# Kernel optimization log

Hardware: AMD Instinct MI355X
Metric: run time of the kernel (lower is better)

Reference implementation:

```python
import jax, jax.numpy as jnp
import numpy as np

D_MODEL = 512
BATCH_A = 8192
MAX_MATCHES = 16
N_B = 100000
D_HID = 2 * D_MODEL  # 1024
D_IN = 2 * D_MODEL   # concat([a, mean_b])


def setup_inputs() -> dict:
    key = jax.random.key(0)
    ks = jax.random.split(key, 10)
    table_a_emb = jax.random.normal(ks[0], (BATCH_A, D_MODEL), dtype=jnp.float32)
    table_b_emb = jax.random.normal(ks[1], (N_B, D_MODEL), dtype=jnp.float32)
    # padded neighbor lists; negative values mark padding / no-match
    match_indices = jax.random.randint(ks[2], (BATCH_A, MAX_MATCHES), -5, N_B, dtype=jnp.int64)
    s_in = 1.0 / np.sqrt(D_IN)
    s_h = 1.0 / np.sqrt(D_HID)
    W_in = jax.random.uniform(ks[3], (D_IN, D_HID), jnp.float32, -s_in, s_in)
    b_in = jax.random.uniform(ks[4], (D_HID,), jnp.float32, -s_in, s_in)
    W_h = jax.random.uniform(ks[5], (D_HID, D_HID), jnp.float32, -s_h, s_h)
    b_h = jax.random.uniform(ks[6], (D_HID,), jnp.float32, -s_h, s_h)
    W_out = jax.random.uniform(ks[7], (D_HID, D_MODEL), jnp.float32, -s_h, s_h)
    b_out = jax.random.uniform(ks[8], (D_MODEL,), jnp.float32, -s_h, s_h)
    return {"table_a_emb": table_a_emb, "table_b_emb": table_b_emb,
            "match_indices": match_indices, "W_in": W_in, "b_in": b_in,
            "W_h": W_h, "b_h": b_h, "W_out": W_out, "b_out": b_out}


def reference(table_a_emb, table_b_emb, match_indices, W_in, b_in, W_h, b_h, W_out, b_out):
    mask = match_indices >= 0                                   # [B, M]
    safe_idx = jnp.where(mask, match_indices, 0)
    gathered = table_b_emb[safe_idx] * mask[..., None].astype(table_b_emb.dtype)  # [B, M, D]
    counts = mask.sum(axis=-1)                                  # [B]
    denom = jnp.maximum(counts, 1).astype(table_b_emb.dtype)[:, None]
    agg_b = gathered.sum(axis=1) / denom                        # [B, D] masked mean
    combined = jnp.concatenate([table_a_emb, agg_b], axis=-1)   # [B, 2D]
    h = jax.nn.relu(combined @ W_in + b_in)
    h = jax.nn.relu(h @ W_h + b_h)
    out = h @ W_out + b_out                                     # [B, D]
    # rows with zero valid matches emit zeros, not MLP(concat(a, 0))
    return jnp.where((counts > 0)[:, None], out, jnp.zeros_like(out))
```

## Files before the change

### kernel.cpp

```cpp
#include <hip/hip_runtime.h>

#define DM 512
#define DI 1024
#define MM 16

typedef __attribute__((ext_vector_type(4))) float f32x4;
typedef __attribute__((ext_vector_type(8))) short short8;
typedef __attribute__((ext_vector_type(8))) unsigned short ushort8;

__device__ __forceinline__ unsigned short f2bf(float x) {
  union { float f; unsigned u; } c; c.f = x;
  unsigned r = (c.u + 0x7fffu + ((c.u >> 16) & 1u)) >> 16;
  return (unsigned short)r;
}

__device__ __forceinline__ void gload_lds16(const void* g, void* l) {
  __builtin_amdgcn_global_load_lds(
      (const __attribute__((address_space(1))) unsigned int*)g,
      (__attribute__((address_space(3))) unsigned int*)l, 16, 0, 0);
}

__device__ __forceinline__ void wt_tile(const float* __restrict__ W,
                                        unsigned short* __restrict__ Wt,
                                        int K, int N, int bx, int by,
                                        float (*tile)[33], int tx, int ty) {
  #pragma unroll
  for (int i = ty; i < 32; i += 8)
    tile[i][tx] = W[(size_t)(by + i) * N + bx + tx];
  __syncthreads();
  #pragma unroll
  for (int i = ty; i < 32; i += 8)
    Wt[(size_t)(bx + i) * K + by + tx] = f2bf(tile[tx][i]);
}

__global__ __launch_bounds__(256)
void prep_kernel(const float* __restrict__ Aemb,
                 const float* __restrict__ Bemb,
                 const int* __restrict__ midx,
                 const float* __restrict__ W_in,
                 const float* __restrict__ W_h,
                 const float* __restrict__ W_out,
                 unsigned short* __restrict__ X,
                 int* __restrict__ counts,
                 unsigned short* __restrict__ Wt_in,
                 unsigned short* __restrict__ Wt_h,
                 unsigned short* __restrict__ Wt_out) {
  __shared__ float tile[32][33];
  const int b = blockIdx.x;
  const int tx = threadIdx.x & 31, ty = threadIdx.x >> 5;
  if (b < 1024) {
    wt_tile(W_in, Wt_in, 1024, 1024, (b & 31) * 32, (b >> 5) * 32, tile, tx, ty);
    return;
  } else if (b < 2048) {
    int lb = b - 1024;
    wt_tile(W_h, Wt_h, 1024, 1024, (lb & 31) * 32, (lb >> 5) * 32, tile, tx, ty);
    return;
  } else if (b < 2560) {
    int lb = b - 2048;
    wt_tile(W_out, Wt_out, 1024, 512, (lb & 15) * 32, (lb >> 4) * 32, tile, tx, ty);
    return;
  }
  int row = __builtin_amdgcn_readfirstlane((b - 2560) * 4 + (threadIdx.x >> 6));
  int l = threadIdx.x & 63;
  float acc[8] = {0,0,0,0,0,0,0,0};
  int cnt = 0;
  const int* ip = midx + row * MM;
  #pragma unroll
  for (int m = 0; m < MM; ++m) {
    int id = ip[m];
    if (id >= 0) {
      ++cnt;
      const f32x4* p = (const f32x4*)(Bemb + (size_t)id * DM) + l * 2;
      f32x4 u = p[0], v = p[1];
      acc[0]+=u[0]; acc[1]+=u[1]; acc[2]+=u[2]; acc[3]+=u[3];
      acc[4]+=v[0]; acc[5]+=v[1]; acc[6]+=v[2]; acc[7]+=v[3];
    }
  }
  float inv = 1.0f / (float)(cnt > 0 ? cnt : 1);
  const f32x4* pa = (const f32x4*)(Aemb + (size_t)row * DM) + l * 2;
  f32x4 a0 = pa[0], a1 = pa[1];
  ushort8 va, vb;
  va[0]=f2bf(a0[0]); va[1]=f2bf(a0[1]); va[2]=f2bf(a0[2]); va[3]=f2bf(a0[3]);
  va[4]=f2bf(a1[0]); va[5]=f2bf(a1[1]); va[6]=f2bf(a1[2]); va[7]=f2bf(a1[3]);
  #pragma unroll
  for (int i = 0; i < 8; ++i) vb[i] = f2bf(acc[i] * inv);
  *(ushort8*)(X + (size_t)row * DI + l * 8) = va;
  *(ushort8*)(X + (size_t)row * DI + DM + l * 8) = vb;
  if (l == 0) counts[row] = cnt;
}

__global__ __launch_bounds__(512, 2)
void gemm8_kernel(const unsigned short* __restrict__ A,
                  const unsigned short* __restrict__ Bt,
                  const float* __restrict__ bias,
                  unsigned short* __restrict__ C) {
  extern __shared__ __align__(16) char smem[];
  const int t = threadIdx.x;
  const int l = t & 63, w = t >> 6;
  const int wr = w >> 2, wc = w & 3;
  const int f = blockIdx.y * gridDim.x + blockIdx.x;
  const int swzid = (f & 7) * 32 + (f >> 3);
  const int bx = swzid & 7, by = swzid >> 3;
  const int blockM = by * 256, blockN = bx * 128;
  const unsigned short* __restrict__ Ab = A + (size_t)blockM * 1024;
  const unsigned short* __restrict__ Bb = Bt + (size_t)blockN * 1024;
  const int r = l & 15, ko = (l >> 4) * 8;
  const int swz = (r & 7) << 4;
  const int strow = t >> 3;
  const int stcolh = ((((t & 7) * 16) ^ ((strow & 7) << 4)) >> 1);

  f32x4 acc[8][2];
  #pragma unroll
  for (int m = 0; m < 8; ++m) {
    acc[m][0] = (f32x4){0.f,0.f,0.f,0.f};
    acc[m][1] = (f32x4){0.f,0.f,0.f,0.f};
  }

#define ST_A(BASE, KT, CH)                                                    \
  gload_lds16(Ab + (size_t)((CH)*64 + strow) * 1024 + ((KT)<<6) + stcolh,     \
              smem + (BASE) + (CH)*8192 + t*16);
#define ST_B(BASE, KT, CB)                                                    \
  gload_lds16(Bb + (size_t)((CB)*64 + strow) * 1024 + ((KT)<<6) + stcolh,     \
              smem + (BASE) + 32768 + (CB)*8192 + t*16);
#define ST_QM0B(BASE, KT) { ST_A(BASE,KT,0) ST_A(BASE,KT,2) ST_B(BASE,KT,0) ST_B(BASE,KT,1) }
#define ST_QM1(BASE, KT)  { ST_A(BASE,KT,1) ST_A(BASE,KT,3) }

#define WAIT_VM(N) { asm volatile("s_waitcnt vmcnt(" #N ")" ::: "memory");    \
                     __builtin_amdgcn_sched_barrier(0); }
#define WAIT_LGKM() { asm volatile("s_waitcnt lgkmcnt(0)" ::: "memory");      \
                      __builtin_amdgcn_sched_barrier(0); }
#define BAR() { __builtin_amdgcn_s_barrier();                                 \
                __builtin_amdgcn_sched_barrier(0); }

  short8 aF[4][2], bF[2][2];

#define LDA(MF4, KK, BASE, QM)                                                \
  aF[MF4][KK] = *(const short8*)(smem + (BASE) +                              \
      ((((wr*128 + ((QM)*4+(MF4))*16 + r) * 128) + ((KK)*32 + ko)*2) ^ swz));
#define LDB(NF, KK, BASE)                                                     \
  bF[NF][KK] = *(const short8*)(smem + (BASE) + 32768 +                       \
      ((((wc*32 + (NF)*16 + r) * 128) + ((KK)*32 + ko)*2) ^ swz));

#define MFMA16(QM)                                                            \
  __builtin_amdgcn_s_setprio(1);                                              \
  _Pragma("unroll") for (int mf4 = 0; mf4 < 4; ++mf4)                         \
    _Pragma("unroll") for (int kk = 0; kk < 2; ++kk)                          \
      _Pragma("unroll") for (int nf = 0; nf < 2; ++nf)                        \
        acc[(QM)*4+mf4][nf] = __builtin_amdgcn_mfma_f32_16x16x32_bf16(        \
            aF[mf4][kk], bF[nf][kk], acc[(QM)*4+mf4][nf], 0, 0, 0);           \
  __builtin_amdgcn_s_setprio(0);

#define DS_A(BASE, QM) _Pragma("unroll")                                      \
  for (int mf4 = 0; mf4 < 4; ++mf4) { LDA(mf4,0,BASE,QM) LDA(mf4,1,BASE,QM) }
#define DS_B(BASE) { LDB(0,0,BASE) LDB(0,1,BASE) LDB(1,0,BASE) LDB(1,1,BASE) }

  ST_QM0B(0, 0) ST_QM1(0, 0)
  ST_QM0B(49152, 1) ST_QM1(49152, 1)
  WAIT_VM(8) BAR()

  { DS_A(0,0) DS_B(0)
    WAIT_LGKM() MFMA16(0)
    WAIT_VM(6) BAR() }
  { DS_A(0,1)
    ST_QM0B(0, 2)
    WAIT_LGKM() MFMA16(1)
    WAIT_VM(6) BAR() }

  #pragma unroll 1
  for (int kt = 1; kt <= 13; ++kt) {
    const int bo = (kt & 1) * 49152;
    const int bo2 = bo ^ 49152;
    { DS_A(bo,0) DS_B(bo)
      ST_QM1(bo2, kt+1)
      WAIT_LGKM() MFMA16(0)
      WAIT_VM(6) BAR() }
    { DS_A(bo,1)
      ST_QM0B(bo, kt+2)
      WAIT_LGKM() MFMA16(1)
      WAIT_VM(6) BAR() }
  }

  { DS_A(0,0) DS_B(0)
    ST_QM1(49152, 15)
    WAIT_LGKM() MFMA16(0)
    WAIT_VM(6) BAR() }
  { DS_A(0,1)
    WAIT_LGKM() MFMA16(1)
    WAIT_VM(2) BAR() }
  { DS_A(49152,0) DS_B(49152)
    WAIT_LGKM() MFMA16(0)
    WAIT_VM(0) BAR() }
  { DS_A(49152,1)
    WAIT_LGKM() MFMA16(1) }

#undef ST_A
#undef ST_B
#undef ST_QM0B
#undef ST_QM1
#undef WAIT_VM
#undef WAIT_LGKM
#undef BAR
#undef LDA
#undef LDB
#undef MFMA16
#undef DS_A
#undef DS_B

  float bn2[2];
  bn2[0] = bias[blockN + wc * 32 + r];
  bn2[1] = bias[blockN + wc * 32 + 16 + r];
  const int rowBase = blockM + wr * 128 + (l >> 4) * 4;
  #pragma unroll
  for (int mf = 0; mf < 8; ++mf)
    #pragma unroll
    for (int j = 0; j < 4; ++j) {
      int grow = rowBase + mf * 16 + j;
      #pragma unroll
      for (int nf = 0; nf < 2; ++nf) {
        float v = acc[mf][nf][j] + bn2[nf];
        v = v > 0.f ? v : 0.f;
        C[(size_t)grow * 1024 + blockN + wc * 32 + nf * 16 + r] = f2bf(v);
      }
    }
}

template<int RELU, int FINAL>
__global__ __launch_bounds__(256, 2)
void gemm_kernel(const unsigned short* __restrict__ A, int lda,
                 const unsigned short* __restrict__ Bt, int ldb, int Kext,
                 const float* __restrict__ bias,
                 unsigned short* __restrict__ Cb,
                 float* __restrict__ Cf,
                 const int* __restrict__ counts,
                 int N) {
  __shared__ __align__(16) unsigned short As[128 * 64];
  __shared__ __align__(16) unsigned short Bs[128 * 64];
  const int t = threadIdx.x;
  const int l = t & 63, w = t >> 6;
  const int wr = w >> 1, wc = w & 1;

  const int nwg = gridDim.x * gridDim.y;
  const int wg = blockIdx.y * gridDim.x + blockIdx.x;
  const int swzid = (wg & 7) * (nwg >> 3) + (wg >> 3);
  const int bx = swzid % gridDim.x, by = swzid / gridDim.x;

  const int blockM = by * 128, blockN = bx * 128;
  const unsigned short* Ab = A + (size_t)blockM * lda;
  const unsigned short* Bb = Bt + (size_t)blockN * ldb;

  f32x4 acc[4][4];
  #pragma unroll
  for (int m = 0; m < 4; ++m)
    #pragma unroll
    for (int n = 0; n < 4; ++n) acc[m][n] = (f32x4){0.f, 0.f, 0.f, 0.f};

  int so_row[4], so_col[4];
  #pragma unroll
  for (int c = 0; c < 4; ++c) {
    int o = c * 4096 + t * 16;
    int row = o >> 7;
    int cb = (o & 127) ^ ((row & 7) << 4);
    so_row[c] = row; so_col[c] = cb >> 1;
  }

  const int r = l & 15, ko = (l >> 4) * 8;
  const int swz = (r & 7) << 4;
  const char* Ac = (const char*)As;
  const char* Bc = (const char*)Bs;
  const int NT = Kext >> 6;

  #pragma unroll
  for (int c = 0; c < 4; ++c) {
    gload_lds16(Ab + (size_t)so_row[c] * lda + so_col[c], (char*)As + c * 4096 + w * 1024);
    gload_lds16(Bb + (size_t)so_row[c] * ldb + so_col[c], (char*)Bs + c * 4096 + w * 1024);
  }

  for (int kt = 0; kt < NT; ++kt) {
    __syncthreads();
    #pragma unroll
    for (int kk = 0; kk < 64; kk += 32) {
      short8 aF[4], bF[4];
      #pragma unroll
      for (int m = 0; m < 4; ++m)
        aF[m] = *(const short8*)(Ac + (((wr * 64 + m * 16 + r) * 128 + (kk + ko) * 2) ^ swz));
      #pragma unroll
      for (int n = 0; n < 4; ++n)
        bF[n] = *(const short8*)(Bc + (((wc * 64 + n * 16 + r) * 128 + (kk + ko) * 2) ^ swz));
      #pragma unroll
      for (int m = 0; m < 4; ++m)
        #pragma unroll
        for (int n = 0; n < 4; ++n)
          acc[m][n] = __builtin_amdgcn_mfma_f32_16x16x32_bf16(aF[m], bF[n], acc[m][n], 0, 0, 0);
    }
    __syncthreads();
    if (kt + 1 < NT) {
      int k0 = (kt + 1) << 6;
      #pragma unroll
      for (int c = 0; c < 4; ++c) {
        gload_lds16(Ab + (size_t)so_row[c] * lda + k0 + so_col[c], (char*)As + c * 4096 + w * 1024);
        gload_lds16(Bb + (size_t)so_row[c] * ldb + k0 + so_col[c], (char*)Bs + c * 4096 + w * 1024);
      }
    }
  }

  float bn[4];
  #pragma unroll
  for (int n = 0; n < 4; ++n) bn[n] = bias[blockN + wc * 64 + n * 16 + r];
  const int rowBase = blockM + wr * 64 + (l >> 4) * 4;
  #pragma unroll
  for (int m = 0; m < 4; ++m) {
    #pragma unroll
    for (int jj = 0; jj < 4; ++jj) {
      int grow = rowBase + m * 16 + jj;
      if (FINAL) {
        float cm = (counts[grow] > 0) ? 1.0f : 0.0f;
        #pragma unroll
        for (int n = 0; n < 4; ++n) {
          float v = (acc[m][n][jj] + bn[n]) * cm;
          Cf[(size_t)grow * N + blockN + wc * 64 + n * 16 + r] = v;
        }
      } else {
        #pragma unroll
        for (int n = 0; n < 4; ++n) {
          float v = acc[m][n][jj] + bn[n];
          if (RELU) v = v > 0.f ? v : 0.f;
          Cb[(size_t)grow * N + blockN + wc * 64 + n * 16 + r] = f2bf(v);
        }
      }
    }
  }
}

extern "C" void kernel_launch(void* const* d_in, const int* in_sizes, int n_in,
                              void* d_out, int out_size, void* d_ws, size_t ws_size,
                              hipStream_t stream) {
  const float* a_emb = (const float*)d_in[0];
  const float* b_emb = (const float*)d_in[1];
  const int*   midx  = (const int*)d_in[2];
  const float* W_in  = (const float*)d_in[3];
  const float* b_in  = (const float*)d_in[4];
  const float* W_h   = (const float*)d_in[5];
  const float* b_h   = (const float*)d_in[6];
  const float* W_out = (const float*)d_in[7];
  const float* b_out = (const float*)d_in[8];
  char* ws = (char*)d_ws;

  unsigned short* X      = (unsigned short*)(ws);
  unsigned short* H1     = (unsigned short*)(ws + 16777216);
  unsigned short* Wt_in  = (unsigned short*)(ws + 33554432);
  unsigned short* Wt_h   = (unsigned short*)(ws + 35651584);
  unsigned short* Wt_out = (unsigned short*)(ws + 37748736);
  int*            counts = (int*)(ws + 38797312);

  (void)hipFuncSetAttribute((const void*)gemm8_kernel,
                            hipFuncAttributeMaxDynamicSharedMemorySize, 98304);

  prep_kernel<<<4608, 256, 0, stream>>>(a_emb, b_emb, midx, W_in, W_h, W_out,
                                        X, counts, Wt_in, Wt_h, Wt_out);

  gemm8_kernel<<<dim3(8, 32), 512, 98304, stream>>>(X,  Wt_in, b_in, H1);
  gemm8_kernel<<<dim3(8, 32), 512, 98304, stream>>>(H1, Wt_h,  b_h,  X);
  gemm_kernel<0, 1><<<dim3(4, 64), 256, 0, stream>>>(X, 1024, Wt_out, 1024, 1024,
                                                     b_out, nullptr, (float*)d_out, counts, 512);
}
```

Measured before the change: 113.2 us.

## Fuse prep and three GEMMs into one cooperative persistent kernel with grid syncs

```diff
diff --git a/kernel.cpp b/kernel.cpp
--- a/kernel.cpp
+++ b/kernel.cpp
@@ -1,4 +1,7 @@
 #include <hip/hip_runtime.h>
+#include <hip/hip_cooperative_groups.h>
+
+namespace cg = cooperative_groups;
 
 #define DM 512
 #define DI 1024
@@ -20,17 +23,288 @@
       (__attribute__((address_space(3))) unsigned int*)l, 16, 0, 0);
 }
 
-__device__ __forceinline__ void wt_tile(const float* __restrict__ W,
-                                        unsigned short* __restrict__ Wt,
-                                        int K, int N, int bx, int by,
-                                        float (*tile)[33], int tx, int ty) {
-  #pragma unroll
-  for (int i = ty; i < 32; i += 8)
-    tile[i][tx] = W[(size_t)(by + i) * N + bx + tx];
-  __syncthreads();
-  #pragma unroll
-  for (int i = ty; i < 32; i += 8)
-    Wt[(size_t)(bx + i) * K + by + tx] = f2bf(tile[tx][i]);
+#define ST_A(BASE, KT, CH)                                                    \
+  gload_lds16(Ab + (size_t)((CH)*64 + strow) * 1024 + ((KT)<<6) + stcolh,     \
+              smem + (BASE) + (CH)*8192 + t*16);
+#define ST_B(BASE, KT, CB)                                                    \
+  gload_lds16(Bb + (size_t)((CB)*64 + strow) * 1024 + ((KT)<<6) + stcolh,     \
+              smem + (BASE) + 32768 + (CB)*8192 + t*16);
+#define ST_QM0B(BASE, KT) { ST_A(BASE,KT,0) ST_A(BASE,KT,2) ST_B(BASE,KT,0) ST_B(BASE,KT,1) }
+#define ST_QM1(BASE, KT)  { ST_A(BASE,KT,1) ST_A(BASE,KT,3) }
+#define WAIT_VM(N) { asm volatile("s_waitcnt vmcnt(" #N ")" ::: "memory");    \
+                     __builtin_amdgcn_sched_barrier(0); }
+#define WAIT_LGKM() { asm volatile("s_waitcnt lgkmcnt(0)" ::: "memory");      \
+                      __builtin_amdgcn_sched_barrier(0); }
+#define BAR() { __builtin_amdgcn_s_barrier();                                 \
+                __builtin_amdgcn_sched_barrier(0); }
+#define LDA(MF4, KK, BASE, QM)                                                \
+  aF[MF4][KK] = *(const short8*)(smem + (BASE) +                              \
+      ((((wr*128 + ((QM)*4+(MF4))*16 + r) * 128) + ((KK)*32 + ko)*2) ^ swz));
+#define LDB(NF, KK, BASE)                                                     \
+  bF[NF][KK] = *(const short8*)(smem + (BASE) + 32768 +                       \
+      ((((wc*32 + (NF)*16 + r) * 128) + ((KK)*32 + ko)*2) ^ swz));
+#define MFMA16(QM)                                                            \
+  __builtin_amdgcn_s_setprio(1);                                              \
+  _Pragma("unroll") for (int mf4 = 0; mf4 < 4; ++mf4)                         \
+    _Pragma("unroll") for (int kk = 0; kk < 2; ++kk)                          \
+      _Pragma("unroll") for (int nf = 0; nf < 2; ++nf)                        \
+        acc[(QM)*4+mf4][nf] = __builtin_amdgcn_mfma_f32_16x16x32_bf16(        \
+            aF[mf4][kk], bF[nf][kk], acc[(QM)*4+mf4][nf], 0, 0, 0);           \
+  __builtin_amdgcn_s_setprio(0);
+#define DS_A(BASE, QM) _Pragma("unroll")                                      \
+  for (int mf4 = 0; mf4 < 4; ++mf4) { LDA(mf4,0,BASE,QM) LDA(mf4,1,BASE,QM) }
+#define DS_B(BASE) { LDB(0,0,BASE) LDB(0,1,BASE) LDB(1,0,BASE) LDB(1,1,BASE) }
+
+__device__ __forceinline__ void gemm256_body(char* smem, int t, int f,
+    const unsigned short* __restrict__ A, const unsigned short* __restrict__ Bt,
+    const float* __restrict__ bias, unsigned short* __restrict__ C) {
+  const int l = t & 63, w = t >> 6;
+  const int wr = w >> 2, wc = w & 3;
+  const int swzid = (f & 7) * 32 + (f >> 3);
+  const int bx = swzid & 7, by = swzid >> 3;
+  const int blockM = by * 256, blockN = bx * 128;
+  const unsigned short* __restrict__ Ab = A + (size_t)blockM * 1024;
+  const unsigned short* __restrict__ Bb = Bt + (size_t)blockN * 1024;
+  const int r = l & 15, ko = (l >> 4) * 8;
+  const int swz = (r & 7) << 4;
+  const int strow = t >> 3;
+  const int stcolh = ((((t & 7) * 16) ^ ((strow & 7) << 4)) >> 1);
+
+  f32x4 acc[8][2];
+  #pragma unroll
+  for (int m = 0; m < 8; ++m) {
+    acc[m][0] = (f32x4){0.f,0.f,0.f,0.f};
+    acc[m][1] = (f32x4){0.f,0.f,0.f,0.f};
+  }
+  short8 aF[4][2], bF[2][2];
+
+  ST_QM0B(0, 0) ST_QM1(0, 0)
+  ST_QM0B(49152, 1) ST_QM1(49152, 1)
+  WAIT_VM(8) BAR()
+  { DS_A(0,0) DS_B(0)
+    WAIT_LGKM() MFMA16(0)
+    WAIT_VM(6) BAR() }
+  { DS_A(0,1)
+    ST_QM0B(0, 2)
+    WAIT_LGKM() MFMA16(1)
+    WAIT_VM(6) BAR() }
+  #pragma unroll 1
+  for (int kt = 1; kt <= 13; ++kt) {
+    const int bo = (kt & 1) * 49152;
+    const int bo2 = bo ^ 49152;
+    { DS_A(bo,0) DS_B(bo)
+      ST_QM1(bo2, kt+1)
+      WAIT_LGKM() MFMA16(0)
+      WAIT_VM(6) BAR() }
+    { DS_A(bo,1)
+      ST_QM0B(bo, kt+2)
+      WAIT_LGKM() MFMA16(1)
+      WAIT_VM(6) BAR() }
+  }
+  { DS_A(0,0) DS_B(0)
+    ST_QM1(49152, 15)
+    WAIT_LGKM() MFMA16(0)
+    WAIT_VM(6) BAR() }
+  { DS_A(0,1)
+    WAIT_LGKM() MFMA16(1)
+    WAIT_VM(2) BAR() }
+  { DS_A(49152,0) DS_B(49152)
+    WAIT_LGKM() MFMA16(0)
+    WAIT_VM(0) BAR() }
+  { DS_A(49152,1)
+    WAIT_LGKM() MFMA16(1) }
+
+  float bn2[2];
+  bn2[0] = bias[blockN + wc * 32 + r];
+  bn2[1] = bias[blockN + wc * 32 + 16 + r];
+  const int rowBase = blockM + wr * 128 + (l >> 4) * 4;
+  #pragma unroll
+  for (int mf = 0; mf < 8; ++mf)
+    #pragma unroll
+    for (int j = 0; j < 4; ++j) {
+      int grow = rowBase + mf * 16 + j;
+      #pragma unroll
+      for (int nf = 0; nf < 2; ++nf) {
+        float v = acc[mf][nf][j] + bn2[nf];
+        v = v > 0.f ? v : 0.f;
+        C[(size_t)grow * 1024 + blockN + wc * 32 + nf * 16 + r] = f2bf(v);
+      }
+    }
+}
+
+#undef ST_A
+#undef ST_B
+#undef ST_QM0B
+#undef ST_QM1
+#undef WAIT_VM
+#undef WAIT_LGKM
+#undef BAR
+#undef LDA
+#undef LDB
+#undef MFMA16
+#undef DS_A
+#undef DS_B
+
+__device__ __forceinline__ void gemm128f_body(char* smem, int t, int f,
+    const unsigned short* __restrict__ A, const unsigned short* __restrict__ Bt,
+    const float* __restrict__ bias, const int* __restrict__ counts,
+    float* __restrict__ Out) {
+  const int l = t & 63, w = t >> 6;
+  const int wr = w >> 2, wc = w & 3;
+  const int swzid = (f & 7) * 32 + (f >> 3);
+  const int bx = swzid & 3, by = swzid >> 2;
+  const int blockM = by * 128, blockN = bx * 128;
+  const unsigned short* __restrict__ Ab = A + (size_t)blockM * 1024;
+  const unsigned short* __restrict__ Bb = Bt + (size_t)blockN * 1024;
+  const int r = l & 15, ko = (l >> 4) * 8;
+  const int swz = (r & 7) << 4;
+
+  int srow[2], scolh[2];
+  #pragma unroll
+  for (int c = 0; c < 2; ++c) {
+    int o = c * 8192 + t * 16;
+    int row = o >> 7;
+    int cb = (o & 127) ^ ((row & 7) << 4);
+    srow[c] = row; scolh[c] = cb >> 1;
+  }
+  f32x4 acc[4][2];
+  #pragma unroll
+  for (int m = 0; m < 4; ++m) {
+    acc[m][0] = (f32x4){0.f,0.f,0.f,0.f};
+    acc[m][1] = (f32x4){0.f,0.f,0.f,0.f};
+  }
+  #pragma unroll
+  for (int c = 0; c < 2; ++c) {
+    gload_lds16(Ab + (size_t)srow[c] * 1024 + scolh[c], smem + c * 8192 + t * 16);
+    gload_lds16(Bb + (size_t)srow[c] * 1024 + scolh[c], smem + 16384 + c * 8192 + t * 16);
+  }
+  for (int kt = 0; kt < 16; ++kt) {
+    __syncthreads();
+    short8 aF[4][2], bF[2][2];
+    #pragma unroll
+    for (int kk = 0; kk < 2; ++kk) {
+      #pragma unroll
+      for (int mf = 0; mf < 4; ++mf)
+        aF[mf][kk] = *(const short8*)(smem + (((wr*64 + mf*16 + r) * 128 + (kk*32 + ko)*2) ^ swz));
+      #pragma unroll
+      for (int nf = 0; nf < 2; ++nf)
+        bF[nf][kk] = *(const short8*)(smem + 16384 + (((wc*32 + nf*16 + r) * 128 + (kk*32 + ko)*2) ^ swz));
+    }
+    #pragma unroll
+    for (int kk = 0; kk < 2; ++kk)
+      #pragma unroll
+      for (int mf = 0; mf < 4; ++mf)
+        #pragma unroll
+        for (int nf = 0; nf < 2; ++nf)
+          acc[mf][nf] = __builtin_amdgcn_mfma_f32_16x16x32_bf16(aF[mf][kk], bF[nf][kk], acc[mf][nf], 0, 0, 0);
+    __syncthreads();
+    if (kt < 15) {
+      int k0 = (kt + 1) << 6;
+      #pragma unroll
+      for (int c = 0; c < 2; ++c) {
+        gload_lds16(Ab + (size_t)srow[c] * 1024 + k0 + scolh[c], smem + c * 8192 + t * 16);
+        gload_lds16(Bb + (size_t)srow[c] * 1024 + k0 + scolh[c], smem + 16384 + c * 8192 + t * 16);
+      }
+    }
+  }
+  float bn2[2];
+  bn2[0] = bias[blockN + wc * 32 + r];
+  bn2[1] = bias[blockN + wc * 32 + 16 + r];
+  const int rowBase = blockM + wr * 64 + (l >> 4) * 4;
+  #pragma unroll
+  for (int mf = 0; mf < 4; ++mf)
+    #pragma unroll
+    for (int j = 0; j < 4; ++j) {
+      int grow = rowBase + mf * 16 + j;
+      float cm = (counts[grow] > 0) ? 1.0f : 0.0f;
+      #pragma unroll
+      for (int nf = 0; nf < 2; ++nf)
+        Out[(size_t)grow * 512 + blockN + wc * 32 + nf * 16 + r] =
+            (acc[mf][nf][j] + bn2[nf]) * cm;
+    }
+}
+
+__device__ __forceinline__ void gather_row(const float* __restrict__ Aemb,
+                                           const float* __restrict__ Bemb,
+                                           const int* __restrict__ midx,
+                                           unsigned short* __restrict__ X,
+                                           int* __restrict__ counts,
+                                           int row, int l) {
+  float acc[8] = {0,0,0,0,0,0,0,0};
+  int cnt = 0;
+  const int* ip = midx + row * MM;
+  #pragma unroll
+  for (int m = 0; m < MM; ++m) {
+    int id = ip[m];
+    if (id >= 0) {
+      ++cnt;
+      const f32x4* p = (const f32x4*)(Bemb + (size_t)id * DM) + l * 2;
+      f32x4 u = p[0], v = p[1];
+      acc[0]+=u[0]; acc[1]+=u[1]; acc[2]+=u[2]; acc[3]+=u[3];
+      acc[4]+=v[0]; acc[5]+=v[1]; acc[6]+=v[2]; acc[7]+=v[3];
+    }
+  }
+  float inv = 1.0f / (float)(cnt > 0 ? cnt : 1);
+  const f32x4* pa = (const f32x4*)(Aemb + (size_t)row * DM) + l * 2;
+  f32x4 a0 = pa[0], a1 = pa[1];
+  ushort8 va, vb;
+  va[0]=f2bf(a0[0]); va[1]=f2bf(a0[1]); va[2]=f2bf(a0[2]); va[3]=f2bf(a0[3]);
+  va[4]=f2bf(a1[0]); va[5]=f2bf(a1[1]); va[6]=f2bf(a1[2]); va[7]=f2bf(a1[3]);
+  #pragma unroll
+  for (int i = 0; i < 8; ++i) vb[i] = f2bf(acc[i] * inv);
+  *(ushort8*)(X + (size_t)row * DI + l * 8) = va;
+  *(ushort8*)(X + (size_t)row * DI + DM + l * 8) = vb;
+  if (l == 0) counts[row] = cnt;
+}
+
+__global__ __launch_bounds__(512, 2)
+void mega_kernel(const float* __restrict__ Aemb, const float* __restrict__ Bemb,
+                 const int* __restrict__ midx,
+                 const float* __restrict__ W_in, const float* __restrict__ W_h,
+                 const float* __restrict__ W_out,
+                 const float* __restrict__ b_in, const float* __restrict__ b_h,
+                 const float* __restrict__ b_out,
+                 unsigned short* __restrict__ X, unsigned short* __restrict__ H1,
+                 unsigned short* __restrict__ Wt_in, unsigned short* __restrict__ Wt_h,
+                 unsigned short* __restrict__ Wt_out,
+                 int* __restrict__ counts, float* __restrict__ Out) {
+  extern __shared__ __align__(16) char smem[];
+  const int t = threadIdx.x;
+  const int blk = blockIdx.x;
+
+  {
+    float (*ftile)[33] = (float(*)[33])smem;
+    const int tx = t & 31, ty = t >> 5;
+    #pragma unroll 1
+    for (int i = 0; i < 10; ++i) {
+      int T = blk * 10 + i;
+      const float* W; unsigned short* Wt; int N, bxx, byy;
+      if (T < 1024)      { W = W_in;  Wt = Wt_in;  N = 1024; bxx = (T & 31) * 32;  byy = (T >> 5) * 32; }
+      else if (T < 2048) { int lb = T - 1024; W = W_h;  Wt = Wt_h;  N = 1024; bxx = (lb & 31) * 32; byy = (lb >> 5) * 32; }
+      else               { int lb = T - 2048; W = W_out; Wt = Wt_out; N = 512; bxx = (lb & 15) * 32; byy = (lb >> 4) * 32; }
+      #pragma unroll
+      for (int i2 = ty; i2 < 32; i2 += 16)
+        ftile[i2][tx] = W[(size_t)(byy + i2) * N + bxx + tx];
+      __syncthreads();
+      #pragma unroll
+      for (int i2 = ty; i2 < 32; i2 += 16)
+        Wt[(size_t)(bxx + i2) * 1024 + byy + tx] = f2bf(ftile[tx][i2]);
+      __syncthreads();
+    }
+  }
+  {
+    const int w8 = t >> 6, l = t & 63;
+    #pragma unroll 1
+    for (int q = 0; q < 4; ++q)
+      gather_row(Aemb, Bemb, midx, X, counts, blk * 32 + w8 * 4 + q, l);
+  }
+
+  cg::this_grid().sync();
+  gemm256_body(smem, t, blk, X, Wt_in, b_in, H1);
+  cg::this_grid().sync();
+  gemm256_body(smem, t, blk, H1, Wt_h, b_h, X);
+  cg::this_grid().sync();
+  gemm128f_body(smem, t, blk, X, Wt_out, b_out, counts, Out);
 }
 
 __global__ __launch_bounds__(256)
@@ -48,45 +322,22 @@
   __shared__ float tile[32][33];
   const int b = blockIdx.x;
   const int tx = threadIdx.x & 31, ty = threadIdx.x >> 5;
-  if (b < 1024) {
-    wt_tile(W_in, Wt_in, 1024, 1024, (b & 31) * 32, (b >> 5) * 32, tile, tx, ty);
+  if (b < 2560) {
+    const float* W; unsigned short* Wt; int N, bxx, byy;
+    if (b < 1024)      { W = W_in;  Wt = Wt_in;  N = 1024; bxx = (b & 31) * 32;  byy = (b >> 5) * 32; }
+    else if (b < 2048) { int lb = b - 1024; W = W_h;  Wt = Wt_h;  N = 1024; bxx = (lb & 31) * 32; byy = (lb >> 5) * 32; }
+    else               { int lb = b - 2048; W = W_out; Wt = Wt_out; N = 512; bxx = (lb & 15) * 32; byy = (lb >> 4) * 32; }
+    #pragma unroll
+    for (int i = ty; i < 32; i += 8)
+      tile[i][tx] = W[(size_t)(byy + i) * N + bxx + tx];
+    __syncthreads();
+    #pragma unroll
+    for (int i = ty; i < 32; i += 8)
+      Wt[(size_t)(bxx + i) * 1024 + byy + tx] = f2bf(tile[tx][i]);
     return;
-  } else if (b < 2048) {
-    int lb = b - 1024;
-    wt_tile(W_h, Wt_h, 1024, 1024, (lb & 31) * 32, (lb >> 5) * 32, tile, tx, ty);
-    return;
-  } else if (b < 2560) {
-    int lb = b - 2048;
-    wt_tile(W_out, Wt_out, 1024, 512, (lb & 15) * 32, (lb >> 4) * 32, tile, tx, ty);
-    return;
-  }
-  int row = __builtin_amdgcn_readfirstlane((b - 2560) * 4 + (threadIdx.x >> 6));
-  int l = threadIdx.x & 63;
-  float acc[8] = {0,0,0,0,0,0,0,0};
-  int cnt = 0;
-  const int* ip = midx + row * MM;
-  #pragma unroll
-  for (int m = 0; m < MM; ++m) {
-    int id = ip[m];
-    if (id >= 0) {
-      ++cnt;
-      const f32x4* p = (const f32x4*)(Bemb + (size_t)id * DM) + l * 2;
-      f32x4 u = p[0], v = p[1];
-      acc[0]+=u[0]; acc[1]+=u[1]; acc[2]+=u[2]; acc[3]+=u[3];
-      acc[4]+=v[0]; acc[5]+=v[1]; acc[6]+=v[2]; acc[7]+=v[3];
-    }
-  }
-  float inv = 1.0f / (float)(cnt > 0 ? cnt : 1);
-  const f32x4* pa = (const f32x4*)(Aemb + (size_t)row * DM) + l * 2;
-  f32x4 a0 = pa[0], a1 = pa[1];
-  ushort8 va, vb;
-  va[0]=f2bf(a0[0]); va[1]=f2bf(a0[1]); va[2]=f2bf(a0[2]); va[3]=f2bf(a0[3]);
-  va[4]=f2bf(a1[0]); va[5]=f2bf(a1[1]); va[6]=f2bf(a1[2]); va[7]=f2bf(a1[3]);
-  #pragma unroll
-  for (int i = 0; i < 8; ++i) vb[i] = f2bf(acc[i] * inv);
-  *(ushort8*)(X + (size_t)row * DI + l * 8) = va;
-  *(ushort8*)(X + (size_t)row * DI + DM + l * 8) = vb;
-  if (l == 0) counts[row] = cnt;
+  }
+  int row = (b - 2560) * 4 + (threadIdx.x >> 6);
+  gather_row(Aemb, Bemb, midx, X, counts, row, threadIdx.x & 63);
 }
 
 __global__ __launch_bounds__(512, 2)
@@ -95,240 +346,17 @@
                   const float* __restrict__ bias,
                   unsigned short* __restrict__ C) {
   extern __shared__ __align__(16) char smem[];
-  const int t = threadIdx.x;
-  const int l = t & 63, w = t >> 6;
-  const int wr = w >> 2, wc = w & 3;
-  const int f = blockIdx.y * gridDim.x + blockIdx.x;
-  const int swzid = (f & 7) * 32 + (f >> 3);
-  const int bx = swzid & 7, by = swzid >> 3;
-  const int blockM = by * 256, blockN = bx * 128;
-  const unsigned short* __restrict__ Ab = A + (size_t)blockM * 1024;
-  const unsigned short* __restrict__ Bb = Bt + (size_t)blockN * 1024;
-  const int r = l & 15, ko = (l >> 4) * 8;
-  const int swz = (r & 7) << 4;
-  const int strow = t >> 3;
-  const int stcolh = ((((t & 7) * 16) ^ ((strow & 7) << 4)) >> 1);
-
-  f32x4 acc[8][2];
-  #pragma unroll
-  for (int m = 0; m < 8; ++m) {
-    acc[m][0] = (f32x4){0.f,0.f,0.f,0.f};
-    acc[m][1] = (f32x4){0.f,0.f,0.f,0.f};
-  }
-
-#define ST_A(BASE, KT, CH)                                                    \
-  gload_lds16(Ab + (size_t)((CH)*64 + strow) * 1024 + ((KT)<<6) + stcolh,     \
-              smem + (BASE) + (CH)*8192 + t*16);
-#define ST_B(BASE, KT, CB)                                                    \
-  gload_lds16(Bb + (size_t)((CB)*64 + strow) * 1024 + ((KT)<<6) + stcolh,     \
-              smem + (BASE) + 32768 + (CB)*8192 + t*16);
-#define ST_QM0B(BASE, KT) { ST_A(BASE,KT,0) ST_A(BASE,KT,2) ST_B(BASE,KT,0) ST_B(BASE,KT,1) }
-#define ST_QM1(BASE, KT)  { ST_A(BASE,KT,1) ST_A(BASE,KT,3) }
-
-#define WAIT_VM(N) { asm volatile("s_waitcnt vmcnt(" #N ")" ::: "memory");    \
-                     __builtin_amdgcn_sched_barrier(0); }
-#define WAIT_LGKM() { asm volatile("s_waitcnt lgkmcnt(0)" ::: "memory");      \
-                      __builtin_amdgcn_sched_barrier(0); }
-#define BAR() { __builtin_amdgcn_s_barrier();                                 \
-                __builtin_amdgcn_sched_barrier(0); }
-
-  short8 aF[4][2], bF[2][2];
-
-#define LDA(MF4, KK, BASE, QM)                                                \
-  aF[MF4][KK] = *(const short8*)(smem + (BASE) +                              \
-      ((((wr*128 + ((QM)*4+(MF4))*16 + r) * 128) + ((KK)*32 + ko)*2) ^ swz));
-#define LDB(NF, KK, BASE)                                                     \
-  bF[NF][KK] = *(const short8*)(smem + (BASE) + 32768 +                       \
-      ((((wc*32 + (NF)*16 + r) * 128) + ((KK)*32 + ko)*2) ^ swz));
-
-#define MFMA16(QM)                                                            \
-  __builtin_amdgcn_s_setprio(1);                                              \
-  _Pragma("unroll") for (int mf4 = 0; mf4 < 4; ++mf4)                         \
-    _Pragma("unroll") for (int kk = 0; kk < 2; ++kk)                          \
-      _Pragma("unroll") for (int nf = 0; nf < 2; ++nf)                        \
-        acc[(QM)*4+mf4][nf] = __builtin_amdgcn_mfma_f32_16x16x32_bf16(        \
-            aF[mf4][kk], bF[nf][kk], acc[(QM)*4+mf4][nf], 0, 0, 0);           \
-  __builtin_amdgcn_s_setprio(0);
-
-#define DS_A(BASE, QM) _Pragma("unroll")                                      \
-  for (int mf4 = 0; mf4 < 4; ++mf4) { LDA(mf4,0,BASE,QM) LDA(mf4,1,BASE,QM) }
-#define DS_B(BASE) { LDB(0,0,BASE) LDB(0,1,BASE) LDB(1,0,BASE) LDB(1,1,BASE) }
-
-  ST_QM0B(0, 0) ST_QM1(0, 0)
-  ST_QM0B(49152, 1) ST_QM1(49152, 1)
-  WAIT_VM(8) BAR()
-
-  { DS_A(0,0) DS_B(0)
-    WAIT_LGKM() MFMA16(0)
-    WAIT_VM(6) BAR() }
-  { DS_A(0,1)
-    ST_QM0B(0, 2)
-    WAIT_LGKM() MFMA16(1)
-    WAIT_VM(6) BAR() }
-
-  #pragma unroll 1
-  for (int kt = 1; kt <= 13; ++kt) {
-    const int bo = (kt & 1) * 49152;
-    const int bo2 = bo ^ 49152;
-    { DS_A(bo,0) DS_B(bo)
-      ST_QM1(bo2, kt+1)
-      WAIT_LGKM() MFMA16(0)
-      WAIT_VM(6) BAR() }
-    { DS_A(bo,1)
-      ST_QM0B(bo, kt+2)
-      WAIT_LGKM() MFMA16(1)
-      WAIT_VM(6) BAR() }
-  }
-
-  { DS_A(0,0) DS_B(0)
-    ST_QM1(49152, 15)
-    WAIT_LGKM() MFMA16(0)
-    WAIT_VM(6) BAR() }
-  { DS_A(0,1)
-    WAIT_LGKM() MFMA16(1)
-    WAIT_VM(2) BAR() }
-  { DS_A(49152,0) DS_B(49152)
-    WAIT_LGKM() MFMA16(0)
-    WAIT_VM(0) BAR() }
-  { DS_A(49152,1)
-    WAIT_LGKM() MFMA16(1) }
-
-#undef ST_A
-#undef ST_B
-#undef ST_QM0B
-#undef ST_QM1
-#undef WAIT_VM
-#undef WAIT_LGKM
-#undef BAR
-#undef LDA
-#undef LDB
-#undef MFMA16
-#undef DS_A
-#undef DS_B
-
-  float bn2[2];
-  bn2[0] = bias[blockN + wc * 32 + r];
-  bn2[1] = bias[blockN + wc * 32 + 16 + r];
-  const int rowBase = blockM + wr * 128 + (l >> 4) * 4;
-  #pragma unroll
-  for (int mf = 0; mf < 8; ++mf)
-    #pragma unroll
-    for (int j = 0; j < 4; ++j) {
-      int grow = rowBase + mf * 16 + j;
-      #pragma unroll
-      for (int nf = 0; nf < 2; ++nf) {
-        float v = acc[mf][nf][j] + bn2[nf];
-        v = v > 0.f ? v : 0.f;
-        C[(size_t)grow * 1024 + blockN + wc * 32 + nf * 16 + r] = f2bf(v);
-      }
-    }
-}
-
-template<int RELU, int FINAL>
-__global__ __launch_bounds__(256, 2)
-void gemm_kernel(const unsigned short* __restrict__ A, int lda,
-                 const unsigned short* __restrict__ Bt, int ldb, int Kext,
-                 const float* __restrict__ bias,
-                 unsigned short* __restrict__ Cb,
-                 float* __restrict__ Cf,
-                 const int* __restrict__ counts,
-                 int N) {
-  __shared__ __align__(16) unsigned short As[128 * 64];
-  __shared__ __align__(16) unsigned short Bs[128 * 64];
-  const int t = threadIdx.x;
-  const int l = t & 63, w = t >> 6;
-  const int wr = w >> 1, wc = w & 1;
-
-  const int nwg = gridDim.x * gridDim.y;
-  const int wg = blockIdx.y * gridDim.x + blockIdx.x;
-  const int swzid = (wg & 7) * (nwg >> 3) + (wg >> 3);
-  const int bx = swzid % gridDim.x, by = swzid / gridDim.x;
-
-  const int blockM = by * 128, blockN = bx * 128;
-  const unsigned short* Ab = A + (size_t)blockM * lda;
-  const unsigned short* Bb = Bt + (size_t)blockN * ldb;
-
-  f32x4 acc[4][4];
-  #pragma unroll
-  for (int m = 0; m < 4; ++m)
-    #pragma unroll
-    for (int n = 0; n < 4; ++n) acc[m][n] = (f32x4){0.f, 0.f, 0.f, 0.f};
-
-  int so_row[4], so_col[4];
-  #pragma unroll
-  for (int c = 0; c < 4; ++c) {
-    int o = c * 4096 + t * 16;
-    int row = o >> 7;
-    int cb = (o & 127) ^ ((row & 7) << 4);
-    so_row[c] = row; so_col[c] = cb >> 1;
-  }
-
-  const int r = l & 15, ko = (l >> 4) * 8;
-  const int swz = (r & 7) << 4;
-  const char* Ac = (const char*)As;
-  const char* Bc = (const char*)Bs;
-  const int NT = Kext >> 6;
-
-  #pragma unroll
-  for (int c = 0; c < 4; ++c) {
-    gload_lds16(Ab + (size_t)so_row[c] * lda + so_col[c], (char*)As + c * 4096 + w * 1024);
-    gload_lds16(Bb + (size_t)so_row[c] * ldb + so_col[c], (char*)Bs + c * 4096 + w * 1024);
-  }
-
-  for (int kt = 0; kt < NT; ++kt) {
-    __syncthreads();
-    #pragma unroll
-    for (int kk = 0; kk < 64; kk += 32) {
-      short8 aF[4], bF[4];
-      #pragma unroll
-      for (int m = 0; m < 4; ++m)
-        aF[m] = *(const short8*)(Ac + (((wr * 64 + m * 16 + r) * 128 + (kk + ko) * 2) ^ swz));
-      #pragma unroll
-      for (int n = 0; n < 4; ++n)
-        bF[n] = *(const short8*)(Bc + (((wc * 64 + n * 16 + r) * 128 + (kk + ko) * 2) ^ swz));
-      #pragma unroll
-      for (int m = 0; m < 4; ++m)
-        #pragma unroll
-        for (int n = 0; n < 4; ++n)
-          acc[m][n] = __builtin_amdgcn_mfma_f32_16x16x32_bf16(aF[m], bF[n], acc[m][n], 0, 0, 0);
-    }
-    __syncthreads();
-    if (kt + 1 < NT) {
-      int k0 = (kt + 1) << 6;
-      #pragma unroll
-      for (int c = 0; c < 4; ++c) {
-        gload_lds16(Ab + (size_t)so_row[c] * lda + k0 + so_col[c], (char*)As + c * 4096 + w * 1024);
-        gload_lds16(Bb + (size_t)so_row[c] * ldb + k0 + so_col[c], (char*)Bs + c * 4096 + w * 1024);
-      }
-    }
-  }
-
-  float bn[4];
-  #pragma unroll
-  for (int n = 0; n < 4; ++n) bn[n] = bias[blockN + wc * 64 + n * 16 + r];
-  const int rowBase = blockM + wr * 64 + (l >> 4) * 4;
-  #pragma unroll
-  for (int m = 0; m < 4; ++m) {
-    #pragma unroll
-    for (int jj = 0; jj < 4; ++jj) {
-      int grow = rowBase + m * 16 + jj;
-      if (FINAL) {
-        float cm = (counts[grow] > 0) ? 1.0f : 0.0f;
-        #pragma unroll
-        for (int n = 0; n < 4; ++n) {
-          float v = (acc[m][n][jj] + bn[n]) * cm;
-          Cf[(size_t)grow * N + blockN + wc * 64 + n * 16 + r] = v;
-        }
-      } else {
-        #pragma unroll
-        for (int n = 0; n < 4; ++n) {
-          float v = acc[m][n][jj] + bn[n];
-          if (RELU) v = v > 0.f ? v : 0.f;
-          Cb[(size_t)grow * N + blockN + wc * 64 + n * 16 + r] = f2bf(v);
-        }
-      }
-    }
-  }
+  gemm256_body(smem, threadIdx.x, (int)blockIdx.x, A, Bt, bias, C);
+}
+
+__global__ __launch_bounds__(512, 2)
+void g3_kernel(const unsigned short* __restrict__ A,
+               const unsigned short* __restrict__ Bt,
+               const float* __restrict__ bias,
+               const int* __restrict__ counts,
+               float* __restrict__ Out) {
+  extern __shared__ __align__(16) char smem[];
+  gemm128f_body(smem, threadIdx.x, (int)blockIdx.x, A, Bt, bias, counts, Out);
 }
 
 extern "C" void kernel_launch(void* const* d_in, const int* in_sizes, int n_in,
@@ -351,15 +379,26 @@
   unsigned short* Wt_h   = (unsigned short*)(ws + 35651584);
   unsigned short* Wt_out = (unsigned short*)(ws + 37748736);
   int*            counts = (int*)(ws + 38797312);
-
+  float*          outp   = (float*)d_out;
+
+  (void)hipFuncSetAttribute((const void*)mega_kernel,
+                            hipFuncAttributeMaxDynamicSharedMemorySize, 98304);
   (void)hipFuncSetAttribute((const void*)gemm8_kernel,
                             hipFuncAttributeMaxDynamicSharedMemorySize, 98304);
 
-  prep_kernel<<<4608, 256, 0, stream>>>(a_emb, b_emb, midx, W_in, W_h, W_out,
-                                        X, counts, Wt_in, Wt_h, Wt_out);
-
-  gemm8_kernel<<<dim3(8, 32), 512, 98304, stream>>>(X,  Wt_in, b_in, H1);
-  gemm8_kernel<<<dim3(8, 32), 512, 98304, stream>>>(H1, Wt_h,  b_h,  X);
-  gemm_kernel<0, 1><<<dim3(4, 64), 256, 0, stream>>>(X, 1024, Wt_out, 1024, 1024,
-                                                     b_out, nullptr, (float*)d_out, counts, 512);
-}
+  void* kargs[] = { (void*)&a_emb, (void*)&b_emb, (void*)&midx,
+                    (void*)&W_in, (void*)&W_h, (void*)&W_out,
+                    (void*)&b_in, (void*)&b_h, (void*)&b_out,
+                    (void*)&X, (void*)&H1, (void*)&Wt_in, (void*)&Wt_h,
+                    (void*)&Wt_out, (void*)&counts, (void*)&outp };
+  hipError_t e = hipLaunchCooperativeKernel((const void*)mega_kernel,
+                                            dim3(256), dim3(512), kargs,
+                                            98304u, stream);
+  if (e != hipSuccess) {
+    prep_kernel<<<4608, 256, 0, stream>>>(a_emb, b_emb, midx, W_in, W_h, W_out,
+                                          X, counts, Wt_in, Wt_h, Wt_out);
+    gemm8_kernel<<<256, 512, 98304, stream>>>(X,  Wt_in, b_in, H1);
+    gemm8_kernel<<<256, 512, 98304, stream>>>(H1, Wt_h,  b_h,  X);
+    g3_kernel<<<256, 512, 32768, stream>>>(X, Wt_out, b_out, counts, outp);
+  }
+}
```

New measurement: 231.9 us. 2.05x slower.
